# Kernel tuning notes

Hardware: AMD Instinct MI355X
Metric: run time of the kernel (lower is better)

The kernel has to match this reference:

```python
import jax, jax.numpy as jnp
import numpy as np

B, NNODE, FIN, FOUT = 64, 512, 64, 64

def setup_inputs() -> dict:
    key = jax.random.key(0)
    ks = jax.random.split(key, 8)
    stdW = 1.0 / np.sqrt(FIN)
    stdA = 1.0 / np.sqrt(FOUT)
    return {
        "X": jax.random.normal(ks[0], (B, NNODE, FIN), dtype=jnp.float32),
        "A": jax.random.uniform(ks[1], (B, NNODE, NNODE), dtype=jnp.float32),
        "N": jax.random.randint(ks[2], (B,), 1, NNODE + 1, dtype=jnp.int64),
        "W": jax.random.uniform(ks[3], (FIN, FOUT), jnp.float32, -stdW, stdW),
        "a": jax.random.uniform(ks[4], (FOUT, FOUT), jnp.float32, -stdA, stdA),
        "bias_W": jax.random.uniform(ks[5], (FOUT,), jnp.float32, -stdW, stdW),
        "bias_a": jax.random.uniform(ks[6], (NNODE,), jnp.float32, -1.0 / np.sqrt(NNODE), 1.0 / np.sqrt(NNODE)),
    }

def reference(X, A, N, W, a, bias_W, bias_a):
    # A_ = A + identity on the top-left n_atoms block (only diagonal entries)
    idx = jnp.arange(A.shape[1])
    diag_mask = (idx[None, :] < N[:, None]).astype(A.dtype)  # [B, n]
    A_ = A + jnp.einsum('bn,nm->bnm', diag_mask, jnp.eye(A.shape[1], dtype=A.dtype))
    # XW: [B, n, F_out]
    XW = jnp.einsum('bnc,cd->bnd', X, W)
    # buf[a,j,k] = sum_i a[i,j] * XW^T[a,j,k]  (einsum 'ij,ajk->ajk')
    col_sum = a.sum(axis=0)  # [F_out]
    XWT = jnp.swapaxes(XW, 1, 2)  # [B, F_out, n]
    buf = col_sum[None, :, None] * XWT
    Z = jnp.einsum('bif,bfk->bik', XW, buf) + bias_a  # [B, n, n] + [n] broadcast on last dim
    att = jnp.tanh(jnp.einsum('bij,bjk->bik', A_, Z))
    H = jnp.einsum('bij,bjd->bid', att, XW) + bias_W
    return H
```

## Files before the change

kernel.cpp:

```cpp
#include <hip/hip_runtime.h>

#define BB 64
#define NN 512
#define FD 64

typedef short bf16x8 __attribute__((ext_vector_type(8)));
typedef float f32x4 __attribute__((ext_vector_type(4)));

__device__ __forceinline__ unsigned short f2bf(float f){
    unsigned u = __builtin_bit_cast(unsigned, f);
    u += 0x7fffu + ((u >> 16) & 1u);
    return (unsigned short)(u >> 16);
}
__device__ __forceinline__ float bf2f(unsigned short h){
    unsigned u = ((unsigned)h) << 16;
    return __builtin_bit_cast(float, u);
}
__device__ __forceinline__ float fast_tanh(float x){
    float e = __expf(2.0f * x);
    return 1.0f - 2.0f * __builtin_amdgcn_rcpf(e + 1.0f);
}
__device__ __forceinline__ bf16x8 pack8(float4 a, float4 b){
    bf16x8 r;
    r[0]=(short)f2bf(a.x); r[1]=(short)f2bf(a.y); r[2]=(short)f2bf(a.z); r[3]=(short)f2bf(a.w);
    r[4]=(short)f2bf(b.x); r[5]=(short)f2bf(b.y); r[6]=(short)f2bf(b.z); r[7]=(short)f2bf(b.w);
    return r;
}

__global__ __launch_bounds__(256) void k_xw(const float* __restrict__ X,
                                            const float* __restrict__ W,
                                            const float* __restrict__ a,
                                            float* __restrict__ colsum,
                                            unsigned short* __restrict__ XWh,
                                            unsigned short* __restrict__ XWt){
    __shared__ float Wf[64][68];
    __shared__ float cpart[4][64];
    __shared__ unsigned short Xl[64][72];
    __shared__ unsigned short Wtl[64][72];
    __shared__ unsigned short Cl[64][72];
    __shared__ unsigned short ClT[64][72];
    int t = threadIdx.x;
    int row0 = blockIdx.x * 64;
    int r = t >> 2, c0 = (t & 3) * 16;
    {
        const float4* srcW = (const float4*)&W[r*64 + c0];
        #pragma unroll
        for (int q = 0; q < 4; q++) *(float4*)&Wf[r][c0 + q*4] = srcW[q];
        const float4* srcX = (const float4*)&X[(row0 + r)*FD + c0];
        #pragma unroll
        for (int q = 0; q < 4; q++){
            float4 v = srcX[q];
            ushort4 h; h.x=f2bf(v.x); h.y=f2bf(v.y); h.z=f2bf(v.z); h.w=f2bf(v.w);
            *(ushort4*)&Xl[r][c0 + q*4] = h;
        }
    }
    if (blockIdx.x == 0){
        int d = t & 63, part = t >> 6;
        float s = 0.f;
        #pragma unroll
        for (int i = 0; i < 16; i++) s += a[(part*16 + i)*64 + d];
        cpart[part][d] = s;
    }
    __syncthreads();
    #pragma unroll
    for (int q = 0; q < 4; q++){
        ushort4 o;
        #pragma unroll
        for (int jj = 0; jj < 4; jj++)
            ((unsigned short*)&o)[jj] = f2bf(Wf[c0 + q*4 + jj][r]);
        *(ushort4*)&Wtl[r][c0 + q*4] = o;
    }
    if (blockIdx.x == 0 && t < 64)
        colsum[t] = cpart[0][t] + cpart[1][t] + cpart[2][t] + cpart[3][t];
    __syncthreads();
    int lane = t & 63, w = t >> 6, l15 = lane & 15, quad = lane >> 4;
    f32x4 acc[4] = {{0,0,0,0},{0,0,0,0},{0,0,0,0},{0,0,0,0}};
    #pragma unroll
    for (int ks = 0; ks < 2; ks++){
        bf16x8 af = *(const bf16x8*)&Xl[w*16 + l15][ks*32 + quad*8];
        #pragma unroll
        for (int nt = 0; nt < 4; nt++){
            bf16x8 bfr = *(const bf16x8*)&Wtl[nt*16 + l15][ks*32 + quad*8];
            acc[nt] = __builtin_amdgcn_mfma_f32_16x16x32_bf16(af, bfr, acc[nt], 0, 0, 0);
        }
    }
    #pragma unroll
    for (int nt = 0; nt < 4; nt++)
        #pragma unroll
        for (int rg = 0; rg < 4; rg++){
            unsigned short hb = f2bf(acc[nt][rg]);
            Cl [w*16 + quad*4 + rg][nt*16 + l15] = hb;
            ClT[nt*16 + l15][w*16 + quad*4 + rg] = hb;
        }
    __syncthreads();
    int b = blockIdx.x >> 3, n0 = (blockIdx.x & 7) * 64;
    {
        uint4 v0 = *(const uint4*)&Cl[r][c0];
        uint4 v1 = *(const uint4*)&Cl[r][c0 + 8];
        *(uint4*)&XWh[(row0 + r)*FD + c0]     = v0;
        *(uint4*)&XWh[(row0 + r)*FD + c0 + 8] = v1;
    }
    {
        uint4 v0 = *(const uint4*)&ClT[r][c0];
        uint4 v1 = *(const uint4*)&ClT[r][c0 + 8];
        *(uint4*)&XWt[(b*64 + r)*NN + n0 + c0]     = v0;
        *(uint4*)&XWt[(b*64 + r)*NN + n0 + c0 + 8] = v1;
    }
}

__global__ __launch_bounds__(512, 1) void k_fused(const float* __restrict__ A,
                                               const unsigned short* __restrict__ XWh,
                                               const unsigned short* __restrict__ XWt,
                                               const float* __restrict__ colsum,
                                               const int* __restrict__ Ni,
                                               const float* __restrict__ bias_a,
                                               const float* __restrict__ bias_W,
                                               float* __restrict__ H){
    __shared__ unsigned short XWtL[64][520];
    __shared__ unsigned short XWhL[512][72];
    __shared__ unsigned short Pl[8][16][72];
    __shared__ float bl[512];
    __shared__ float csl[64];
    int t = threadIdx.x;
    int b = blockIdx.x, it2 = blockIdx.y;
    int lane = t & 63, w = t >> 6, l15 = lane & 15, quad = lane >> 4;
    int tl = w >> 2, st = w & 3;
    int i0 = (it2 + 4*tl) * 64;
    int Nb = (Ni[1] == 0) ? Ni[2*b] : Ni[b];
    const unsigned short* XWtb = XWt + b*64*NN;
    const unsigned short* XWhb = XWh + b*NN*FD;
    const float* Arow = A + (size_t)(b*NN + i0 + st*16 + l15)*NN + quad*8;

    float4 pa[4][2];
    #pragma unroll
    for (int s = 0; s < 4; s++){
        pa[s][0] = *(const float4*)&Arow[s*32];
        pa[s][1] = *(const float4*)&Arow[s*32 + 4];
    }
    #pragma unroll
    for (int q = 0; q < 8; q++){
        int m = t + 512*q;
        *(uint4*)&XWtL[m >> 6][(m & 63)*8] = *(const uint4*)&XWtb[(m >> 6)*NN + (m & 63)*8];
    }
    #pragma unroll
    for (int q = 0; q < 8; q++){
        int m = t + 512*q;
        *(uint4*)&XWhL[m >> 3][(m & 7)*8] = *(const uint4*)&XWhb[(m >> 3)*FD + (m & 7)*8];
    }
    bl[t] = bias_a[t];
    if (t < 64) csl[t] = colsum[t];
    __syncthreads();

    f32x4 acc[4] = {{0,0,0,0},{0,0,0,0},{0,0,0,0},{0,0,0,0}};
    float rs = 0.f;
    #pragma unroll
    for (int s = 0; s < 16; s++){
        float4 v0 = pa[s & 3][0], v1 = pa[s & 3][1];
        if (s < 12){
            pa[s & 3][0] = *(const float4*)&Arow[(s + 4)*32];
            pa[s & 3][1] = *(const float4*)&Arow[(s + 4)*32 + 4];
        }
        rs += (v0.x + v0.y) + (v0.z + v0.w) + (v1.x + v1.y) + (v1.z + v1.w);
        bf16x8 af = pack8(v0, v1);
        #pragma unroll
        for (int nt = 0; nt < 4; nt++){
            bf16x8 bfr = *(const bf16x8*)&XWtL[nt*16 + l15][s*32 + quad*8];
            acc[nt] = __builtin_amdgcn_mfma_f32_16x16x32_bf16(af, bfr, acc[nt], 0, 0, 0);
        }
    }
    #pragma unroll
    for (int nt = 0; nt < 4; nt++)
        #pragma unroll
        for (int rg = 0; rg < 4; rg++){
            int i = i0 + st*16 + quad*4 + rg;
            if (i < Nb) acc[nt][rg] += bf2f(XWhL[i][nt*16 + l15]);
        }
    float rsum = rs;
    rsum += __shfl_xor(rsum, 16);
    rsum += __shfl_xor(rsum, 32);
    #pragma unroll
    for (int nt = 0; nt < 4; nt++){
        float cs = csl[nt*16 + l15];
        #pragma unroll
        for (int rg = 0; rg < 4; rg++)
            Pl[w][quad*4 + rg][nt*16 + l15] = f2bf(acc[nt][rg] * cs);
    }
    asm volatile("s_waitcnt lgkmcnt(0)" ::: "memory");
    __builtin_amdgcn_sched_barrier(0);
    bf16x8 maf[2];
    maf[0] = *(const bf16x8*)&Pl[w][l15][quad*8];
    maf[1] = *(const bf16x8*)&Pl[w][l15][32 + quad*8];
    float rs_r[4];
    #pragma unroll
    for (int rg = 0; rg < 4; rg++){
        int i = i0 + st*16 + quad*4 + rg;
        rs_r[rg] = __shfl(rsum, quad*4 + rg) + ((i < Nb) ? 1.f : 0.f);
    }

    f32x4 hacc[4] = {{0,0,0,0},{0,0,0,0},{0,0,0,0},{0,0,0,0}};
    #pragma unroll
    for (int jt = 0; jt < 8; jt++){
        #pragma unroll
        for (int nt = 0; nt < 4; nt++){
            float bv = bl[jt*64 + nt*16 + l15];
            f32x4 arg = { rs_r[0]*bv, rs_r[1]*bv, rs_r[2]*bv, rs_r[3]*bv };
            #pragma unroll
            for (int ks = 0; ks < 2; ks++){
                bf16x8 bfr = *(const bf16x8*)&XWhL[jt*64 + nt*16 + l15][ks*32 + quad*8];
                arg = __builtin_amdgcn_mfma_f32_16x16x32_bf16(maf[ks], bfr, arg, 0, 0, 0);
            }
            #pragma unroll
            for (int rg = 0; rg < 4; rg++)
                Pl[w][quad*4 + rg][nt*16 + l15] = f2bf(fast_tanh(arg[rg]));
        }
        asm volatile("s_waitcnt lgkmcnt(0)" ::: "memory");
        __builtin_amdgcn_sched_barrier(0);
        #pragma unroll
        for (int ks = 0; ks < 2; ks++){
            bf16x8 paf = *(const bf16x8*)&Pl[w][l15][ks*32 + quad*8];
            #pragma unroll
            for (int dt = 0; dt < 4; dt++){
                bf16x8 bfr = *(const bf16x8*)&XWtL[dt*16 + l15][jt*64 + ks*32 + quad*8];
                hacc[dt] = __builtin_amdgcn_mfma_f32_16x16x32_bf16(paf, bfr, hacc[dt], 0, 0, 0);
            }
        }
    }
    #pragma unroll
    for (int dt = 0; dt < 4; dt++){
        float bw = bias_W[dt*16 + l15];
        #pragma unroll
        for (int rg = 0; rg < 4; rg++)
            H[(size_t)(b*NN + i0 + st*16 + quad*4 + rg)*FD + dt*16 + l15] = hacc[dt][rg] + bw;
    }
}

extern "C" void kernel_launch(void* const* d_in, const int* in_sizes, int n_in,
                              void* d_out, int out_size, void* d_ws, size_t ws_size,
                              hipStream_t stream){
    const float* X      = (const float*)d_in[0];
    const float* A      = (const float*)d_in[1];
    const int*   N      = (const int*)  d_in[2];
    const float* W      = (const float*)d_in[3];
    const float* a      = (const float*)d_in[4];
    const float* bias_W = (const float*)d_in[5];
    const float* bias_a = (const float*)d_in[6];
    float* H = (float*)d_out;
    char* ws = (char*)d_ws;

    unsigned short* XWh    = (unsigned short*)(ws);
    unsigned short* XWt    = (unsigned short*)(ws + (4u<<20));
    float*          colsum = (float*)(ws + (8u<<20));

    k_xw   <<<BB * NN / 64, 256, 0, stream>>>(X, W, a, colsum, XWh, XWt);
    k_fused<<<dim3(BB, 4), 512, 0, stream>>>(A, XWh, XWt, colsum, N, bias_a, bias_W, H);
}
```

Measured before the change: 128.0 us.

## Fuse XW projection into main kernel and swizzle XW shared layout

Result: no change. 126.9 us (-0.8%).

```diff
diff --git a/kernel.cpp b/kernel.cpp
--- a/kernel.cpp
+++ b/kernel.cpp
@@ -27,98 +27,51 @@
     return r;
 }
 
-__global__ __launch_bounds__(256) void k_xw(const float* __restrict__ X,
-                                            const float* __restrict__ W,
-                                            const float* __restrict__ a,
-                                            float* __restrict__ colsum,
-                                            unsigned short* __restrict__ XWh,
-                                            unsigned short* __restrict__ XWt){
-    __shared__ float Wf[64][68];
+__global__ __launch_bounds__(256) void k_prep(const float* __restrict__ W,
+                                              const float* __restrict__ a,
+                                              float* __restrict__ colsum,
+                                              unsigned short* __restrict__ Wt){
+    __shared__ float Wl[64][68];
     __shared__ float cpart[4][64];
-    __shared__ unsigned short Xl[64][72];
-    __shared__ unsigned short Wtl[64][72];
-    __shared__ unsigned short Cl[64][72];
-    __shared__ unsigned short ClT[64][72];
     int t = threadIdx.x;
-    int row0 = blockIdx.x * 64;
+    int d = t & 63, part = t >> 6;
+    float s = 0.f;
+    #pragma unroll
+    for (int i = 0; i < 16; i++) s += a[(part*16 + i)*64 + d];
+    cpart[part][d] = s;
     int r = t >> 2, c0 = (t & 3) * 16;
     {
-        const float4* srcW = (const float4*)&W[r*64 + c0];
-        #pragma unroll
-        for (int q = 0; q < 4; q++) *(float4*)&Wf[r][c0 + q*4] = srcW[q];
-        const float4* srcX = (const float4*)&X[(row0 + r)*FD + c0];
-        #pragma unroll
-        for (int q = 0; q < 4; q++){
-            float4 v = srcX[q];
-            ushort4 h; h.x=f2bf(v.x); h.y=f2bf(v.y); h.z=f2bf(v.z); h.w=f2bf(v.w);
-            *(ushort4*)&Xl[r][c0 + q*4] = h;
-        }
-    }
-    if (blockIdx.x == 0){
-        int d = t & 63, part = t >> 6;
-        float s = 0.f;
-        #pragma unroll
-        for (int i = 0; i < 16; i++) s += a[(part*16 + i)*64 + d];
-        cpart[part][d] = s;
+        const float4* src = (const float4*)&W[r*64 + c0];
+        #pragma unroll
+        for (int q = 0; q < 4; q++) *(float4*)&Wl[r][c0 + q*4] = src[q];
     }
     __syncthreads();
+    if (part == 0) colsum[d] = cpart[0][d] + cpart[1][d] + cpart[2][d] + cpart[3][d];
     #pragma unroll
     for (int q = 0; q < 4; q++){
         ushort4 o;
         #pragma unroll
         for (int jj = 0; jj < 4; jj++)
-            ((unsigned short*)&o)[jj] = f2bf(Wf[c0 + q*4 + jj][r]);
-        *(ushort4*)&Wtl[r][c0 + q*4] = o;
-    }
-    if (blockIdx.x == 0 && t < 64)
-        colsum[t] = cpart[0][t] + cpart[1][t] + cpart[2][t] + cpart[3][t];
-    __syncthreads();
-    int lane = t & 63, w = t >> 6, l15 = lane & 15, quad = lane >> 4;
-    f32x4 acc[4] = {{0,0,0,0},{0,0,0,0},{0,0,0,0},{0,0,0,0}};
-    #pragma unroll
-    for (int ks = 0; ks < 2; ks++){
-        bf16x8 af = *(const bf16x8*)&Xl[w*16 + l15][ks*32 + quad*8];
-        #pragma unroll
-        for (int nt = 0; nt < 4; nt++){
-            bf16x8 bfr = *(const bf16x8*)&Wtl[nt*16 + l15][ks*32 + quad*8];
-            acc[nt] = __builtin_amdgcn_mfma_f32_16x16x32_bf16(af, bfr, acc[nt], 0, 0, 0);
-        }
-    }
-    #pragma unroll
-    for (int nt = 0; nt < 4; nt++)
-        #pragma unroll
-        for (int rg = 0; rg < 4; rg++){
-            unsigned short hb = f2bf(acc[nt][rg]);
-            Cl [w*16 + quad*4 + rg][nt*16 + l15] = hb;
-            ClT[nt*16 + l15][w*16 + quad*4 + rg] = hb;
-        }
-    __syncthreads();
-    int b = blockIdx.x >> 3, n0 = (blockIdx.x & 7) * 64;
-    {
-        uint4 v0 = *(const uint4*)&Cl[r][c0];
-        uint4 v1 = *(const uint4*)&Cl[r][c0 + 8];
-        *(uint4*)&XWh[(row0 + r)*FD + c0]     = v0;
-        *(uint4*)&XWh[(row0 + r)*FD + c0 + 8] = v1;
-    }
-    {
-        uint4 v0 = *(const uint4*)&ClT[r][c0];
-        uint4 v1 = *(const uint4*)&ClT[r][c0 + 8];
-        *(uint4*)&XWt[(b*64 + r)*NN + n0 + c0]     = v0;
-        *(uint4*)&XWt[(b*64 + r)*NN + n0 + c0 + 8] = v1;
-    }
-}
-
-__global__ __launch_bounds__(512, 1) void k_fused(const float* __restrict__ A,
-                                               const unsigned short* __restrict__ XWh,
-                                               const unsigned short* __restrict__ XWt,
+            ((unsigned short*)&o)[jj] = f2bf(Wl[c0 + q*4 + jj][r]);
+        *(ushort4*)&Wt[r*64 + c0 + q*4] = o;
+    }
+}
+
+#define XWH_BYTE(n, f)  ((unsigned)(n)*128u + (((((unsigned)(f) >> 3) ^ ((unsigned)(n) & 7u)) & 7u) << 4) + (((unsigned)(f) & 7u) << 1))
+#define XWH_B128(n, f0) ((unsigned)(n)*128u + (((((unsigned)(f0) >> 3) ^ ((unsigned)(n) & 7u)) & 7u) << 4))
+
+__global__ __launch_bounds__(512, 1) void k_fused(const float* __restrict__ X,
+                                               const float* __restrict__ A,
+                                               const unsigned short* __restrict__ Wt,
                                                const float* __restrict__ colsum,
                                                const int* __restrict__ Ni,
                                                const float* __restrict__ bias_a,
                                                const float* __restrict__ bias_W,
                                                float* __restrict__ H){
     __shared__ unsigned short XWtL[64][520];
-    __shared__ unsigned short XWhL[512][72];
+    __shared__ unsigned short XWhL[512*64];
     __shared__ unsigned short Pl[8][16][72];
+    __shared__ unsigned short Wtl[64][72];
     __shared__ float bl[512];
     __shared__ float csl[64];
     int t = threadIdx.x;
@@ -127,28 +80,51 @@
     int tl = w >> 2, st = w & 3;
     int i0 = (it2 + 4*tl) * 64;
     int Nb = (Ni[1] == 0) ? Ni[2*b] : Ni[b];
-    const unsigned short* XWtb = XWt + b*64*NN;
-    const unsigned short* XWhb = XWh + b*NN*FD;
+    const float* Xb = X + (size_t)b*NN*FD;
     const float* Arow = A + (size_t)(b*NN + i0 + st*16 + l15)*NN + quad*8;
 
+    float4 xv[8][2];
+    #pragma unroll
+    for (int rt = 0; rt < 4; rt++)
+        #pragma unroll
+        for (int ks = 0; ks < 2; ks++){
+            const float* p = &Xb[(w*64 + rt*16 + l15)*FD + ks*32 + quad*8];
+            xv[rt*2 + ks][0] = *(const float4*)p;
+            xv[rt*2 + ks][1] = *(const float4*)(p + 4);
+        }
     float4 pa[4][2];
     #pragma unroll
     for (int s = 0; s < 4; s++){
         pa[s][0] = *(const float4*)&Arow[s*32];
         pa[s][1] = *(const float4*)&Arow[s*32 + 4];
     }
-    #pragma unroll
-    for (int q = 0; q < 8; q++){
-        int m = t + 512*q;
-        *(uint4*)&XWtL[m >> 6][(m & 63)*8] = *(const uint4*)&XWtb[(m >> 6)*NN + (m & 63)*8];
-    }
-    #pragma unroll
-    for (int q = 0; q < 8; q++){
-        int m = t + 512*q;
-        *(uint4*)&XWhL[m >> 3][(m & 7)*8] = *(const uint4*)&XWhb[(m >> 3)*FD + (m & 7)*8];
-    }
+    *(uint4*)&Wtl[t >> 3][(t & 7)*8] = *(const uint4*)&Wt[(t >> 3)*64 + (t & 7)*8];
     bl[t] = bias_a[t];
     if (t < 64) csl[t] = colsum[t];
+    __syncthreads();
+
+    #pragma unroll
+    for (int rt = 0; rt < 4; rt++){
+        f32x4 c[4] = {{0,0,0,0},{0,0,0,0},{0,0,0,0},{0,0,0,0}};
+        #pragma unroll
+        for (int ks = 0; ks < 2; ks++){
+            bf16x8 af = pack8(xv[rt*2 + ks][0], xv[rt*2 + ks][1]);
+            #pragma unroll
+            for (int nt = 0; nt < 4; nt++){
+                bf16x8 bfr = *(const bf16x8*)&Wtl[nt*16 + l15][ks*32 + quad*8];
+                c[nt] = __builtin_amdgcn_mfma_f32_16x16x32_bf16(af, bfr, c[nt], 0, 0, 0);
+            }
+        }
+        #pragma unroll
+        for (int nt = 0; nt < 4; nt++)
+            #pragma unroll
+            for (int rg = 0; rg < 4; rg++){
+                unsigned short hb = f2bf(c[nt][rg]);
+                int n = w*64 + rt*16 + quad*4 + rg, f = nt*16 + l15;
+                *(unsigned short*)((char*)XWhL + XWH_BYTE(n, f)) = hb;
+                XWtL[f][n] = hb;
+            }
+    }
     __syncthreads();
 
     f32x4 acc[4] = {{0,0,0,0},{0,0,0,0},{0,0,0,0},{0,0,0,0}};
@@ -173,7 +149,8 @@
         #pragma unroll
         for (int rg = 0; rg < 4; rg++){
             int i = i0 + st*16 + quad*4 + rg;
-            if (i < Nb) acc[nt][rg] += bf2f(XWhL[i][nt*16 + l15]);
+            if (i < Nb)
+                acc[nt][rg] += bf2f(*(const unsigned short*)((const char*)XWhL + XWH_BYTE(i, nt*16 + l15)));
         }
     float rsum = rs;
     rsum += __shfl_xor(rsum, 16);
@@ -202,11 +179,12 @@
     for (int jt = 0; jt < 8; jt++){
         #pragma unroll
         for (int nt = 0; nt < 4; nt++){
-            float bv = bl[jt*64 + nt*16 + l15];
+            int j = jt*64 + nt*16 + l15;
+            float bv = bl[j];
             f32x4 arg = { rs_r[0]*bv, rs_r[1]*bv, rs_r[2]*bv, rs_r[3]*bv };
             #pragma unroll
             for (int ks = 0; ks < 2; ks++){
-                bf16x8 bfr = *(const bf16x8*)&XWhL[jt*64 + nt*16 + l15][ks*32 + quad*8];
+                bf16x8 bfr = *(const bf16x8*)((const char*)XWhL + XWH_B128(j, ks*32 + quad*8));
                 arg = __builtin_amdgcn_mfma_f32_16x16x32_bf16(maf[ks], bfr, arg, 0, 0, 0);
             }
             #pragma unroll
@@ -247,10 +225,9 @@
     float* H = (float*)d_out;
     char* ws = (char*)d_ws;
 
-    unsigned short* XWh    = (unsigned short*)(ws);
-    unsigned short* XWt    = (unsigned short*)(ws + (4u<<20));
-    float*          colsum = (float*)(ws + (8u<<20));
-
-    k_xw   <<<BB * NN / 64, 256, 0, stream>>>(X, W, a, colsum, XWh, XWt);
-    k_fused<<<dim3(BB, 4), 512, 0, stream>>>(A, XWh, XWt, colsum, N, bias_a, bias_W, H);
-}
+    unsigned short* Wt     = (unsigned short*)(ws);
+    float*          colsum = (float*)(ws + 8192);
+
+    k_prep <<<1, 256, 0, stream>>>(W, a, colsum, Wt);
+    k_fused<<<dim3(BB, 4), 512, 0, stream>>>(X, A, Wt, colsum, N, bias_a, bias_W, H);
+}
```

## Split fused kernel into two smaller kernels reading operands directly from global memory

Applied to the files above, without the earlier changes.

Result: slower. 166.3 us (+29.9%).

```diff
diff --git a/kernel.cpp b/kernel.cpp
--- a/kernel.cpp
+++ b/kernel.cpp
@@ -15,6 +15,9 @@
 __device__ __forceinline__ float bf2f(unsigned short h){
     unsigned u = ((unsigned)h) << 16;
     return __builtin_bit_cast(float, u);
+}
+__device__ __forceinline__ unsigned pkbf2(float a, float b){
+    return (unsigned)f2bf(a) | ((unsigned)f2bf(b) << 16);
 }
 __device__ __forceinline__ float fast_tanh(float x){
     float e = __expf(2.0f * x);
@@ -108,129 +111,126 @@
     }
 }
 
-__global__ __launch_bounds__(512, 1) void k_fused(const float* __restrict__ A,
-                                               const unsigned short* __restrict__ XWh,
-                                               const unsigned short* __restrict__ XWt,
-                                               const float* __restrict__ colsum,
-                                               const int* __restrict__ Ni,
-                                               const float* __restrict__ bias_a,
-                                               const float* __restrict__ bias_W,
-                                               float* __restrict__ H){
-    __shared__ unsigned short XWtL[64][520];
-    __shared__ unsigned short XWhL[512][72];
-    __shared__ unsigned short Pl[8][16][72];
-    __shared__ float bl[512];
-    __shared__ float csl[64];
+__global__ __launch_bounds__(256, 6) void k_phaseA(const float* __restrict__ A,
+                                                   const unsigned short* __restrict__ XWh,
+                                                   const unsigned short* __restrict__ XWt,
+                                                   const float* __restrict__ colsum,
+                                                   const int* __restrict__ Ni,
+                                                   unsigned short* __restrict__ M,
+                                                   float* __restrict__ rowsum){
     int t = threadIdx.x;
-    int b = blockIdx.x, it2 = blockIdx.y;
+    int b = blockIdx.x, it = blockIdx.y;
+    int i0 = it * 64;
     int lane = t & 63, w = t >> 6, l15 = lane & 15, quad = lane >> 4;
-    int tl = w >> 2, st = w & 3;
-    int i0 = (it2 + 4*tl) * 64;
     int Nb = (Ni[1] == 0) ? Ni[2*b] : Ni[b];
-    const unsigned short* XWtb = XWt + b*64*NN;
-    const unsigned short* XWhb = XWh + b*NN*FD;
-    const float* Arow = A + (size_t)(b*NN + i0 + st*16 + l15)*NN + quad*8;
-
-    float4 pa[4][2];
-    #pragma unroll
-    for (int s = 0; s < 4; s++){
+    const float* Arow = A + (size_t)(b*NN + i0 + w*16 + l15)*NN + quad*8;
+    const unsigned short* XWtb = XWt + (size_t)b*64*NN;
+    const unsigned short* XWhb = XWh + (size_t)b*NN*FD;
+
+    float4 pa[3][2];
+    #pragma unroll
+    for (int s = 0; s < 3; s++){
         pa[s][0] = *(const float4*)&Arow[s*32];
         pa[s][1] = *(const float4*)&Arow[s*32 + 4];
     }
-    #pragma unroll
-    for (int q = 0; q < 8; q++){
-        int m = t + 512*q;
-        *(uint4*)&XWtL[m >> 6][(m & 63)*8] = *(const uint4*)&XWtb[(m >> 6)*NN + (m & 63)*8];
-    }
-    #pragma unroll
-    for (int q = 0; q < 8; q++){
-        int m = t + 512*q;
-        *(uint4*)&XWhL[m >> 3][(m & 7)*8] = *(const uint4*)&XWhb[(m >> 3)*FD + (m & 7)*8];
-    }
-    bl[t] = bias_a[t];
-    if (t < 64) csl[t] = colsum[t];
-    __syncthreads();
-
     f32x4 acc[4] = {{0,0,0,0},{0,0,0,0},{0,0,0,0},{0,0,0,0}};
     float rs = 0.f;
     #pragma unroll
     for (int s = 0; s < 16; s++){
-        float4 v0 = pa[s & 3][0], v1 = pa[s & 3][1];
-        if (s < 12){
-            pa[s & 3][0] = *(const float4*)&Arow[(s + 4)*32];
-            pa[s & 3][1] = *(const float4*)&Arow[(s + 4)*32 + 4];
+        float4 v0 = pa[s % 3][0], v1 = pa[s % 3][1];
+        if (s < 13){
+            pa[s % 3][0] = *(const float4*)&Arow[(s + 3)*32];
+            pa[s % 3][1] = *(const float4*)&Arow[(s + 3)*32 + 4];
         }
         rs += (v0.x + v0.y) + (v0.z + v0.w) + (v1.x + v1.y) + (v1.z + v1.w);
         bf16x8 af = pack8(v0, v1);
         #pragma unroll
         for (int nt = 0; nt < 4; nt++){
-            bf16x8 bfr = *(const bf16x8*)&XWtL[nt*16 + l15][s*32 + quad*8];
-            acc[nt] = __builtin_amdgcn_mfma_f32_16x16x32_bf16(af, bfr, acc[nt], 0, 0, 0);
-        }
-    }
-    #pragma unroll
-    for (int nt = 0; nt < 4; nt++)
-        #pragma unroll
-        for (int rg = 0; rg < 4; rg++){
-            int i = i0 + st*16 + quad*4 + rg;
-            if (i < Nb) acc[nt][rg] += bf2f(XWhL[i][nt*16 + l15]);
-        }
+            bf16x8 xa = *(const bf16x8*)&XWtb[(nt*16 + l15)*NN + s*32 + quad*8];
+            acc[nt] = __builtin_amdgcn_mfma_f32_16x16x32_bf16(xa, af, acc[nt], 0, 0, 0);
+        }
+    }
+    int irow = i0 + w*16 + l15;
+    bool dg = irow < Nb;
     float rsum = rs;
     rsum += __shfl_xor(rsum, 16);
     rsum += __shfl_xor(rsum, 32);
+    if (lane < 16){
+        int i = i0 + w*16 + lane;
+        rowsum[b*NN + i] = rsum + ((i < Nb) ? 1.f : 0.f);
+    }
     #pragma unroll
     for (int nt = 0; nt < 4; nt++){
-        float cs = csl[nt*16 + l15];
-        #pragma unroll
-        for (int rg = 0; rg < 4; rg++)
-            Pl[w][quad*4 + rg][nt*16 + l15] = f2bf(acc[nt][rg] * cs);
-    }
-    asm volatile("s_waitcnt lgkmcnt(0)" ::: "memory");
-    __builtin_amdgcn_sched_barrier(0);
+        float4 cs4 = *(const float4*)&colsum[nt*16 + quad*4];
+        ushort4 dh = *(const ushort4*)&XWhb[(size_t)irow*FD + nt*16 + quad*4];
+        float m0 = (acc[nt][0] + (dg ? bf2f(dh.x) : 0.f)) * cs4.x;
+        float m1 = (acc[nt][1] + (dg ? bf2f(dh.y) : 0.f)) * cs4.y;
+        float m2 = (acc[nt][2] + (dg ? bf2f(dh.z) : 0.f)) * cs4.z;
+        float m3 = (acc[nt][3] + (dg ? bf2f(dh.w) : 0.f)) * cs4.w;
+        uint2 pk = { pkbf2(m0, m1), pkbf2(m2, m3) };
+        *(uint2*)&M[((size_t)b*NN + irow)*FD + nt*16 + quad*4] = pk;
+    }
+}
+
+__global__ __launch_bounds__(256, 6) void k_phaseB(const unsigned short* __restrict__ XWh,
+                                                   const unsigned short* __restrict__ XWt,
+                                                   const unsigned short* __restrict__ M,
+                                                   const float* __restrict__ rowsum,
+                                                   const float* __restrict__ bias_a,
+                                                   const float* __restrict__ bias_W,
+                                                   float* __restrict__ H){
+    __shared__ unsigned short Pl[4][16][72];
+    int t = threadIdx.x;
+    int b = blockIdx.x, it = blockIdx.y;
+    int i0 = it * 64;
+    int lane = t & 63, w = t >> 6, l15 = lane & 15, quad = lane >> 4;
+    int irow = i0 + w*16 + l15;
+    const unsigned short* XWtb = XWt + (size_t)b*64*NN;
+    const unsigned short* XWhb = XWh + (size_t)b*NN*FD;
+    const unsigned short* Mrow = M + ((size_t)b*NN + irow)*FD;
+
     bf16x8 maf[2];
-    maf[0] = *(const bf16x8*)&Pl[w][l15][quad*8];
-    maf[1] = *(const bf16x8*)&Pl[w][l15][32 + quad*8];
-    float rs_r[4];
-    #pragma unroll
-    for (int rg = 0; rg < 4; rg++){
-        int i = i0 + st*16 + quad*4 + rg;
-        rs_r[rg] = __shfl(rsum, quad*4 + rg) + ((i < Nb) ? 1.f : 0.f);
-    }
+    maf[0] = *(const bf16x8*)&Mrow[quad*8];
+    maf[1] = *(const bf16x8*)&Mrow[32 + quad*8];
+    float rsum_l = rowsum[b*NN + irow];
+    float4 bwv[4];
+    #pragma unroll
+    for (int dt = 0; dt < 4; dt++) bwv[dt] = *(const float4*)&bias_W[dt*16 + quad*4];
 
     f32x4 hacc[4] = {{0,0,0,0},{0,0,0,0},{0,0,0,0},{0,0,0,0}};
     #pragma unroll
     for (int jt = 0; jt < 8; jt++){
         #pragma unroll
         for (int nt = 0; nt < 4; nt++){
-            float bv = bl[jt*64 + nt*16 + l15];
-            f32x4 arg = { rs_r[0]*bv, rs_r[1]*bv, rs_r[2]*bv, rs_r[3]*bv };
+            float4 blv = *(const float4*)&bias_a[jt*64 + nt*16 + quad*4];
+            f32x4 arg = { rsum_l*blv.x, rsum_l*blv.y, rsum_l*blv.z, rsum_l*blv.w };
             #pragma unroll
             for (int ks = 0; ks < 2; ks++){
-                bf16x8 bfr = *(const bf16x8*)&XWhL[jt*64 + nt*16 + l15][ks*32 + quad*8];
-                arg = __builtin_amdgcn_mfma_f32_16x16x32_bf16(maf[ks], bfr, arg, 0, 0, 0);
+                bf16x8 xh = *(const bf16x8*)&XWhb[(size_t)(jt*64 + nt*16 + l15)*FD + ks*32 + quad*8];
+                arg = __builtin_amdgcn_mfma_f32_16x16x32_bf16(xh, maf[ks], arg, 0, 0, 0);
             }
-            #pragma unroll
-            for (int rg = 0; rg < 4; rg++)
-                Pl[w][quad*4 + rg][nt*16 + l15] = f2bf(fast_tanh(arg[rg]));
+            uint2 pk = { pkbf2(fast_tanh(arg[0]), fast_tanh(arg[1])),
+                         pkbf2(fast_tanh(arg[2]), fast_tanh(arg[3])) };
+            *(uint2*)&Pl[w][l15][nt*16 + quad*4] = pk;
         }
         asm volatile("s_waitcnt lgkmcnt(0)" ::: "memory");
         __builtin_amdgcn_sched_barrier(0);
         #pragma unroll
         for (int ks = 0; ks < 2; ks++){
-            bf16x8 paf = *(const bf16x8*)&Pl[w][l15][ks*32 + quad*8];
+            bf16x8 pf = *(const bf16x8*)&Pl[w][l15][ks*32 + quad*8];
             #pragma unroll
             for (int dt = 0; dt < 4; dt++){
-                bf16x8 bfr = *(const bf16x8*)&XWtL[dt*16 + l15][jt*64 + ks*32 + quad*8];
-                hacc[dt] = __builtin_amdgcn_mfma_f32_16x16x32_bf16(paf, bfr, hacc[dt], 0, 0, 0);
+                bf16x8 xt = *(const bf16x8*)&XWtb[(size_t)(dt*16 + l15)*NN + jt*64 + ks*32 + quad*8];
+                hacc[dt] = __builtin_amdgcn_mfma_f32_16x16x32_bf16(xt, pf, hacc[dt], 0, 0, 0);
             }
         }
     }
+    float* Hrow = H + (size_t)(b*NN + irow)*FD;
     #pragma unroll
     for (int dt = 0; dt < 4; dt++){
-        float bw = bias_W[dt*16 + l15];
-        #pragma unroll
-        for (int rg = 0; rg < 4; rg++)
-            H[(size_t)(b*NN + i0 + st*16 + quad*4 + rg)*FD + dt*16 + l15] = hacc[dt][rg] + bw;
+        float4 hv = { hacc[dt][0] + bwv[dt].x, hacc[dt][1] + bwv[dt].y,
+                      hacc[dt][2] + bwv[dt].z, hacc[dt][3] + bwv[dt].w };
+        *(float4*)&Hrow[dt*16 + quad*4] = hv;
     }
 }
 
@@ -249,8 +249,11 @@
 
     unsigned short* XWh    = (unsigned short*)(ws);
     unsigned short* XWt    = (unsigned short*)(ws + (4u<<20));
-    float*          colsum = (float*)(ws + (8u<<20));
-
-    k_xw   <<<BB * NN / 64, 256, 0, stream>>>(X, W, a, colsum, XWh, XWt);
-    k_fused<<<dim3(BB, 4), 512, 0, stream>>>(A, XWh, XWt, colsum, N, bias_a, bias_W, H);
-}
+    unsigned short* M      = (unsigned short*)(ws + (8u<<20));
+    float*          rowsum = (float*)(ws + (12u<<20));
+    float*          colsum = (float*)(ws + (12u<<20) + (128u<<10));
+
+    k_xw    <<<BB * NN / 64, 256, 0, stream>>>(X, W, a, colsum, XWh, XWt);
+    k_phaseA<<<dim3(BB, 8), 256, 0, stream>>>(A, XWh, XWt, colsum, N, M, rowsum);
+    k_phaseB<<<dim3(BB, 8), 256, 0, stream>>>(XWh, XWt, M, rowsum, bias_a, bias_W, H);
+}
```

## Stream A through swizzled LDS double buffer via async global-to-LDS loads

Applied to the files above, without the earlier changes.

Result: no change. 130.3 us (+1.8%).

```diff
diff --git a/kernel.cpp b/kernel.cpp
--- a/kernel.cpp
+++ b/kernel.cpp
@@ -15,6 +15,9 @@
 __device__ __forceinline__ float bf2f(unsigned short h){
     unsigned u = ((unsigned)h) << 16;
     return __builtin_bit_cast(float, u);
+}
+__device__ __forceinline__ unsigned pkbf2(float a, float b){
+    return (unsigned)f2bf(a) | ((unsigned)f2bf(b) << 16);
 }
 __device__ __forceinline__ float fast_tanh(float x){
     float e = __expf(2.0f * x);
@@ -25,6 +28,11 @@
     r[0]=(short)f2bf(a.x); r[1]=(short)f2bf(a.y); r[2]=(short)f2bf(a.z); r[3]=(short)f2bf(a.w);
     r[4]=(short)f2bf(b.x); r[5]=(short)f2bf(b.y); r[6]=(short)f2bf(b.z); r[7]=(short)f2bf(b.w);
     return r;
+}
+__device__ __forceinline__ void gl2lds(const void* g, void* l){
+    __builtin_amdgcn_global_load_lds(
+        (const __attribute__((address_space(1))) unsigned int*)g,
+        (__attribute__((address_space(3))) unsigned int*)l, 16, 0, 0);
 }
 
 __global__ __launch_bounds__(256) void k_xw(const float* __restrict__ X,
@@ -117,8 +125,7 @@
                                                const float* __restrict__ bias_W,
                                                float* __restrict__ H){
     __shared__ unsigned short XWtL[64][520];
-    __shared__ unsigned short XWhL[512][72];
-    __shared__ unsigned short Pl[8][16][72];
+    __shared__ float Abuf[8][2][1024];
     __shared__ float bl[512];
     __shared__ float csl[64];
     int t = threadIdx.x;
@@ -127,110 +134,134 @@
     int tl = w >> 2, st = w & 3;
     int i0 = (it2 + 4*tl) * 64;
     int Nb = (Ni[1] == 0) ? Ni[2*b] : Ni[b];
-    const unsigned short* XWtb = XWt + b*64*NN;
-    const unsigned short* XWhb = XWh + b*NN*FD;
-    const float* Arow = A + (size_t)(b*NN + i0 + st*16 + l15)*NN + quad*8;
-
-    float4 pa[4][2];
-    #pragma unroll
-    for (int s = 0; s < 4; s++){
-        pa[s][0] = *(const float4*)&Arow[s*32];
-        pa[s][1] = *(const float4*)&Arow[s*32 + 4];
-    }
-    #pragma unroll
-    for (int q = 0; q < 8; q++){
-        int m = t + 512*q;
-        *(uint4*)&XWtL[m >> 6][(m & 63)*8] = *(const uint4*)&XWtb[(m >> 6)*NN + (m & 63)*8];
-    }
-    #pragma unroll
-    for (int q = 0; q < 8; q++){
-        int m = t + 512*q;
-        *(uint4*)&XWhL[m >> 3][(m & 7)*8] = *(const uint4*)&XWhb[(m >> 3)*FD + (m & 7)*8];
+    const unsigned short* XWtb = XWt + (size_t)b*64*NN;
+    const unsigned short* XWhb = XWh + (size_t)b*NN*FD;
+
+    #pragma unroll
+    for (int r8 = 0; r8 < 8; r8++){
+        int row = w*8 + r8;
+        gl2lds(&XWtb[(size_t)row*NN + lane*8], &XWtL[row][0]);
     }
     bl[t] = bias_a[t];
     if (t < 64) csl[t] = colsum[t];
     __syncthreads();
 
+    int irow = i0 + st*16 + l15;
+    bool dg = irow < Nb;
+    ushort4 dh[4];
+    #pragma unroll
+    for (int nt = 0; nt < 4; nt++)
+        dh[nt] = *(const ushort4*)&XWhb[(size_t)irow*FD + nt*16 + quad*4];
+
+    const float* Arowbase = A + (size_t)(b*NN + i0 + st*16)*NN;
+    auto issue_chunk = [&](int c){
+        #pragma unroll
+        for (int q = 0; q < 4; q++){
+            int r = q*4 + (lane >> 4);
+            int cc = lane & 15;
+            gl2lds(&Arowbase[(size_t)r*NN + c*64 + ((cc ^ (r & 7)) << 2)],
+                   &Abuf[w][c & 1][q*256]);
+        }
+    };
+    issue_chunk(0);
+    issue_chunk(1);
+
     f32x4 acc[4] = {{0,0,0,0},{0,0,0,0},{0,0,0,0},{0,0,0,0}};
     float rs = 0.f;
     #pragma unroll
-    for (int s = 0; s < 16; s++){
-        float4 v0 = pa[s & 3][0], v1 = pa[s & 3][1];
-        if (s < 12){
-            pa[s & 3][0] = *(const float4*)&Arow[(s + 4)*32];
-            pa[s & 3][1] = *(const float4*)&Arow[(s + 4)*32 + 4];
-        }
-        rs += (v0.x + v0.y) + (v0.z + v0.w) + (v1.x + v1.y) + (v1.z + v1.w);
-        bf16x8 af = pack8(v0, v1);
-        #pragma unroll
-        for (int nt = 0; nt < 4; nt++){
-            bf16x8 bfr = *(const bf16x8*)&XWtL[nt*16 + l15][s*32 + quad*8];
-            acc[nt] = __builtin_amdgcn_mfma_f32_16x16x32_bf16(af, bfr, acc[nt], 0, 0, 0);
-        }
-    }
-    #pragma unroll
-    for (int nt = 0; nt < 4; nt++)
-        #pragma unroll
-        for (int rg = 0; rg < 4; rg++){
-            int i = i0 + st*16 + quad*4 + rg;
-            if (i < Nb) acc[nt][rg] += bf2f(XWhL[i][nt*16 + l15]);
-        }
+    for (int c = 0; c < 8; c++){
+        if (c == 7) asm volatile("s_waitcnt vmcnt(0)" ::: "memory");
+        else        asm volatile("s_waitcnt vmcnt(4)" ::: "memory");
+        __builtin_amdgcn_sched_barrier(0);
+        const float* Ab = &Abuf[w][c & 1][0];
+        #pragma unroll
+        for (int ks2 = 0; ks2 < 2; ks2++){
+            int cc0 = ks2*8 + quad*2;
+            float4 v0 = *(const float4*)&Ab[l15*64 + ((cc0       ^ (l15 & 7)) << 2)];
+            float4 v1 = *(const float4*)&Ab[l15*64 + (((cc0 + 1) ^ (l15 & 7)) << 2)];
+            rs += (v0.x + v0.y) + (v0.z + v0.w) + (v1.x + v1.y) + (v1.z + v1.w);
+            bf16x8 af = pack8(v0, v1);
+            int s = c*2 + ks2;
+            #pragma unroll
+            for (int nt = 0; nt < 4; nt++){
+                bf16x8 xa = *(const bf16x8*)&XWtL[nt*16 + l15][s*32 + quad*8];
+                acc[nt] = __builtin_amdgcn_mfma_f32_16x16x32_bf16(xa, af, acc[nt], 0, 0, 0);
+            }
+        }
+        if (c < 6){
+            asm volatile("s_waitcnt lgkmcnt(0)" ::: "memory");
+            __builtin_amdgcn_sched_barrier(0);
+            issue_chunk(c + 2);
+        }
+    }
     float rsum = rs;
     rsum += __shfl_xor(rsum, 16);
     rsum += __shfl_xor(rsum, 32);
+    float rsum_l = rsum + (dg ? 1.f : 0.f);
+    unsigned short* Ps = (unsigned short*)&Abuf[w][0][0];
     #pragma unroll
     for (int nt = 0; nt < 4; nt++){
-        float cs = csl[nt*16 + l15];
-        #pragma unroll
-        for (int rg = 0; rg < 4; rg++)
-            Pl[w][quad*4 + rg][nt*16 + l15] = f2bf(acc[nt][rg] * cs);
+        float4 cs4 = *(const float4*)&csl[nt*16 + quad*4];
+        float m0 = (acc[nt][0] + (dg ? bf2f(dh[nt].x) : 0.f)) * cs4.x;
+        float m1 = (acc[nt][1] + (dg ? bf2f(dh[nt].y) : 0.f)) * cs4.y;
+        float m2 = (acc[nt][2] + (dg ? bf2f(dh[nt].z) : 0.f)) * cs4.z;
+        float m3 = (acc[nt][3] + (dg ? bf2f(dh[nt].w) : 0.f)) * cs4.w;
+        uint2 pk = { pkbf2(m0, m1), pkbf2(m2, m3) };
+        *(uint2*)&Ps[l15*72 + nt*16 + quad*4] = pk;
     }
     asm volatile("s_waitcnt lgkmcnt(0)" ::: "memory");
     __builtin_amdgcn_sched_barrier(0);
     bf16x8 maf[2];
-    maf[0] = *(const bf16x8*)&Pl[w][l15][quad*8];
-    maf[1] = *(const bf16x8*)&Pl[w][l15][32 + quad*8];
-    float rs_r[4];
-    #pragma unroll
-    for (int rg = 0; rg < 4; rg++){
-        int i = i0 + st*16 + quad*4 + rg;
-        rs_r[rg] = __shfl(rsum, quad*4 + rg) + ((i < Nb) ? 1.f : 0.f);
-    }
-
+    maf[0] = *(const bf16x8*)&Ps[l15*72 + quad*8];
+    maf[1] = *(const bf16x8*)&Ps[l15*72 + 32 + quad*8];
+
+    bf16x8 xcur[8], xnxt[8];
+    #pragma unroll
+    for (int nt = 0; nt < 4; nt++)
+        #pragma unroll
+        for (int ks = 0; ks < 2; ks++)
+            xcur[nt*2 + ks] = *(const bf16x8*)&XWhb[(size_t)(nt*16 + l15)*FD + ks*32 + quad*8];
     f32x4 hacc[4] = {{0,0,0,0},{0,0,0,0},{0,0,0,0},{0,0,0,0}};
     #pragma unroll
     for (int jt = 0; jt < 8; jt++){
+        if (jt < 7){
+            #pragma unroll
+            for (int nt = 0; nt < 4; nt++)
+                #pragma unroll
+                for (int ks = 0; ks < 2; ks++)
+                    xnxt[nt*2 + ks] = *(const bf16x8*)&XWhb[(size_t)((jt+1)*64 + nt*16 + l15)*FD + ks*32 + quad*8];
+        }
         #pragma unroll
         for (int nt = 0; nt < 4; nt++){
-            float bv = bl[jt*64 + nt*16 + l15];
-            f32x4 arg = { rs_r[0]*bv, rs_r[1]*bv, rs_r[2]*bv, rs_r[3]*bv };
-            #pragma unroll
-            for (int ks = 0; ks < 2; ks++){
-                bf16x8 bfr = *(const bf16x8*)&XWhL[jt*64 + nt*16 + l15][ks*32 + quad*8];
-                arg = __builtin_amdgcn_mfma_f32_16x16x32_bf16(maf[ks], bfr, arg, 0, 0, 0);
-            }
-            #pragma unroll
-            for (int rg = 0; rg < 4; rg++)
-                Pl[w][quad*4 + rg][nt*16 + l15] = f2bf(fast_tanh(arg[rg]));
+            float4 blv = *(const float4*)&bl[jt*64 + nt*16 + quad*4];
+            f32x4 arg = { rsum_l*blv.x, rsum_l*blv.y, rsum_l*blv.z, rsum_l*blv.w };
+            arg = __builtin_amdgcn_mfma_f32_16x16x32_bf16(xcur[nt*2 + 0], maf[0], arg, 0, 0, 0);
+            arg = __builtin_amdgcn_mfma_f32_16x16x32_bf16(xcur[nt*2 + 1], maf[1], arg, 0, 0, 0);
+            uint2 pk = { pkbf2(fast_tanh(arg[0]), fast_tanh(arg[1])),
+                         pkbf2(fast_tanh(arg[2]), fast_tanh(arg[3])) };
+            *(uint2*)&Ps[l15*72 + nt*16 + quad*4] = pk;
         }
         asm volatile("s_waitcnt lgkmcnt(0)" ::: "memory");
         __builtin_amdgcn_sched_barrier(0);
         #pragma unroll
         for (int ks = 0; ks < 2; ks++){
-            bf16x8 paf = *(const bf16x8*)&Pl[w][l15][ks*32 + quad*8];
+            bf16x8 pf = *(const bf16x8*)&Ps[l15*72 + ks*32 + quad*8];
             #pragma unroll
             for (int dt = 0; dt < 4; dt++){
-                bf16x8 bfr = *(const bf16x8*)&XWtL[dt*16 + l15][jt*64 + ks*32 + quad*8];
-                hacc[dt] = __builtin_amdgcn_mfma_f32_16x16x32_bf16(paf, bfr, hacc[dt], 0, 0, 0);
+                bf16x8 xt = *(const bf16x8*)&XWtL[dt*16 + l15][jt*64 + ks*32 + quad*8];
+                hacc[dt] = __builtin_amdgcn_mfma_f32_16x16x32_bf16(xt, pf, hacc[dt], 0, 0, 0);
             }
         }
-    }
+        #pragma unroll
+        for (int q = 0; q < 8; q++) xcur[q] = xnxt[q];
+    }
+    float* Hrow = H + (size_t)(b*NN + irow)*FD;
     #pragma unroll
     for (int dt = 0; dt < 4; dt++){
-        float bw = bias_W[dt*16 + l15];
-        #pragma unroll
-        for (int rg = 0; rg < 4; rg++)
-            H[(size_t)(b*NN + i0 + st*16 + quad*4 + rg)*FD + dt*16 + l15] = hacc[dt][rg] + bw;
+        float4 bwv = *(const float4*)&bias_W[dt*16 + quad*4];
+        float4 hv = { hacc[dt][0] + bwv.x, hacc[dt][1] + bwv.y,
+                      hacc[dt][2] + bwv.z, hacc[dt][3] + bwv.w };
+        *(float4*)&Hrow[dt*16 + quad*4] = hv;
     }
 }
 
```
